# Kernel optimization log

Hardware: AMD Instinct MI355X
Metric: run time of the kernel (lower is better)

Reference implementation:

```python
import jax, jax.numpy as jnp
import numpy as np

B, Q, K, D = 16, 2048, 2048, 128
NEG = -1000000.0  # matches torch module's mask fill value (not -inf)


def setup_inputs() -> dict:
    key = jax.random.key(0)
    kq, kk, kv, kl = jax.random.split(key, 4)
    q = jax.random.normal(kq, (B, Q, D), dtype=jnp.float32)
    k = jax.random.normal(kk, (B, K, D), dtype=jnp.float32)
    v = jax.random.normal(kv, (B, K, D), dtype=jnp.float32)
    valid_lens = jax.random.randint(kl, (B, 1), 0, K, dtype=jnp.int32)
    return {"q": q, "k": k, "v": v, "valid_lens": valid_lens}


def reference(q, k, v, valid_lens):
    d = q.shape[-1]
    # scores: (B, Q, K)
    weight = jnp.einsum('bqd,bkd->bqk', q, k) / jnp.sqrt(jnp.asarray(d, q.dtype))
    # mask: key position j valid iff j < valid_len[b]; broadcast over query dim
    mask = jnp.arange(k.shape[1])[None, None, :] < valid_lens[:, :, None]  # (B,1,K)
    weight = jnp.where(mask, weight, NEG)
    score = jax.nn.softmax(weight, axis=-1)
    return jnp.einsum('bqk,bkv->bqv', score, v)
```

## Files before the change

kernel.cpp:

```cpp
#include <hip/hip_runtime.h>

constexpr int NB = 16;
constexpr int NQ = 2048;
constexpr int NK = 2048;
constexpr int ND = 128;
constexpr int KVBLK = 64;
constexpr int NTILE = NK / KVBLK;
constexpr int TILE_USH = KVBLK * ND;
constexpr float SCALE2 = 0.12751744751442557f;

typedef __attribute__((ext_vector_type(4))) float f4;
typedef __attribute__((ext_vector_type(16))) float f32x16;
typedef __attribute__((ext_vector_type(8))) unsigned short us8;
typedef __attribute__((ext_vector_type(8))) __bf16 bf16x8;
typedef __attribute__((ext_vector_type(4))) unsigned int u32x4;

static __device__ __forceinline__ unsigned short f2bf(float f) {
    unsigned u = __builtin_bit_cast(unsigned, f);
    u += 0x7fffu + ((u >> 16) & 1u);
    return (unsigned short)(u >> 16);
}
static __device__ __forceinline__ f4 splat4(float x) { f4 r = {x,x,x,x}; return r; }

static __device__ __forceinline__ float fexp2(float x) {
    float r;
    asm("v_exp_f32 %0, %1" : "=v"(r) : "v"(x));
    return r;
}

static __device__ __forceinline__ void load_lds16(const unsigned short* g, unsigned short* l) {
    __builtin_amdgcn_global_load_lds(
        (const __attribute__((address_space(1))) void*)g,
        (__attribute__((address_space(3))) void*)l,
        16, 0, 0);
}

static __device__ __forceinline__ unsigned cvt_pk_bf16(float lo, float hi) {
    unsigned r;
    asm("v_cvt_pk_bf16_f32 %0, %1, %2" : "=v"(r) : "v"(lo), "v"(hi));
    return r;
}

__global__ __launch_bounds__(256)
void prep_kv5(const float* __restrict__ kg, const float* __restrict__ vg,
              const int* __restrict__ vlen,
              unsigned short* __restrict__ wk, unsigned short* __restrict__ wvt)
{
    const int b   = blockIdx.y;
    const int t   = blockIdx.x;
    const int kv0 = t * KVBLK;

    {
        const int v = vlen[b];
        const int Leff = (v <= 0) ? NK : v;
        if (kv0 >= Leff) return;
    }

    const int t0  = threadIdx.x;

    __shared__ __align__(16) unsigned short vl[64 * 136];

    {
        const int kv = t0 >> 2;
        const int c  = t0 & 3;
        const float* gp = kg + (size_t)(b * NK + kv0 + kv) * ND + c * 32;
        unsigned short* ob = wk + (size_t)(b * NTILE + t) * TILE_USH;
        #pragma unroll
        for (int g = 0; g < 4; ++g) {
            f4 f0 = *(const f4*)(gp + g * 8);
            f4 f1 = *(const f4*)(gp + g * 8 + 4);
            us8 w;
            #pragma unroll
            for (int i = 0; i < 4; ++i) { w[i] = f2bf(f0[i]); w[i+4] = f2bf(f1[i]); }
            const int d0 = c * 32 + g * 8;
            const int f  = (kv >> 5) * 8 + (d0 >> 4);
            const int off = f * 512 + ((d0 >> 3) & 1) * 256 + (kv & 31) * 8;
            *(us8*)(ob + off) = w;
        }
    }
    {
        const int kv = t0 >> 2;
        const int d0 = (t0 & 3) * 32;
        const float* gp = vg + (size_t)(b * NK + kv0 + kv) * ND + d0;
        unsigned short* lb = &vl[kv * 136 + d0];
        #pragma unroll
        for (int g = 0; g < 4; ++g) {
            f4 f0 = *(const f4*)(gp + g * 8);
            f4 f1 = *(const f4*)(gp + g * 8 + 4);
            us8 w;
            #pragma unroll
            for (int i = 0; i < 4; ++i) { w[i] = f2bf(f0[i]); w[i+4] = f2bf(f1[i]); }
            *(us8*)(lb + g * 8) = w;
        }
    }
    __syncthreads();
    {
        unsigned short* ob = wvt + (size_t)(b * NTILE + t) * TILE_USH;
        #pragma unroll
        for (int iter = 0; iter < 4; ++iter) {
            const int cid = iter * 256 + t0;
            const int f   = cid >> 6;
            const int l   = cid & 63;
            const int kb  = (f >> 2) * 16 + (l >> 5) * 8;
            const int d   = (f & 3) * 32 + (l & 31);
            us8 w;
            #pragma unroll
            for (int j = 0; j < 8; ++j) w[j] = vl[(kb + j) * 136 + d];
            *(us8*)(ob + cid * 8) = w;
        }
    }
}

__global__ __launch_bounds__(256, 2)
void attn_fused14(const float* __restrict__ qg, const int* __restrict__ vlen,
                  const unsigned short* __restrict__ wk,
                  const unsigned short* __restrict__ wvt,
                  float* __restrict__ og)
{
    const int bid  = blockIdx.x;
    const int half = bid >> 8;
    const int j    = bid & 255;
    const int rank = half ? (15 - (j & 7)) : (j & 7);
    const int qc   = j >> 3;
    const int q0   = qc * 64;

    int b = 0;
    {
        int Ls[16];
        #pragma unroll
        for (int i = 0; i < 16; ++i) {
            const int v = vlen[i];
            Ls[i] = (v <= 0) ? NK : v;
        }
        #pragma unroll
        for (int bb = 0; bb < 16; ++bb) {
            int r = 0;
            #pragma unroll
            for (int cc = 0; cc < 16; ++cc)
                r += (Ls[cc] > Ls[bb] || (Ls[cc] == Ls[bb] && cc < bb)) ? 1 : 0;
            if (r == rank) b = bb;
        }
    }

    const int tid  = threadIdx.x;
    const int wid  = tid >> 6;
    const int grp  = wid >> 1;
    const int qw   = wid & 1;
    const int lane = tid & 63;
    const int lq   = lane & 31;
    const int hi   = lane >> 5;

    const int L = vlen[b];
    const bool uniform = (L <= 0);
    const int Leff = uniform ? NK : L;
    const int ntiles = (Leff + KVBLK - 1) / KVBLK;
    const int ng    = (ntiles + 1 - grp) >> 1;
    const int niter = (ntiles + 1) >> 1;

    __shared__ __align__(16) unsigned short smem[2][2 * TILE_USH];

    bf16x8 aq[8];
    {
        const float* qp = qg + (size_t)(b * NQ + q0 + qw * 32 + lq) * ND + hi * 8;
        #pragma unroll
        for (int c = 0; c < 8; ++c) {
            f4 f0 = *(const f4*)(qp + c * 16);
            f4 f1 = *(const f4*)(qp + c * 16 + 4);
            us8 u;
            #pragma unroll
            for (int i = 0; i < 4; ++i) {
                u[i]     = f2bf(f0[i] * SCALE2);
                u[i + 4] = f2bf(f1[i] * SCALE2);
            }
            aq[c] = __builtin_bit_cast(bf16x8, u);
        }
    }

    const unsigned short* kbg = wk  + (size_t)b * NTILE * TILE_USH;
    const unsigned short* vbg = wvt + (size_t)b * NTILE * TILE_USH;

    const unsigned short* sbase = qw ? vbg : kbg;
    unsigned short* sdst = &smem[grp][qw * 8192];
    const int s_off = lane * 8;

    float m_r = -__builtin_inff();
    float l_r = 0.f;
    f32x16 accO[4];
    #pragma unroll
    for (int dc = 0; dc < 4; ++dc)
        #pragma unroll
        for (int r = 0; r < 16; ++r) accO[dc][r] = 0.f;

    if (grp < ntiles) {
        const unsigned short* src = sbase + (size_t)grp * TILE_USH + s_off;
        #pragma unroll
        for (int jj = 0; jj < 16; ++jj) load_lds16(src + jj * 512, sdst + jj * 512);
    }
    __syncthreads();

    for (int i = 0; i < niter; ++i) {
        const int tile = 2 * i + grp;
        const unsigned short* kl  = &smem[grp][0];
        const unsigned short* vl2 = &smem[grp][8192];
        const bool act = (i < ng);

        us8 kf[16], vf[16];
        f32x16 sA, sB;
        if (act) {
            #pragma unroll
            for (int c = 0; c < 16; ++c)
                kf[c] = *(const us8*)&kl[c * 512 + lane * 8];
            #pragma unroll
            for (int r = 0; r < 16; ++r) { sA[r] = 0.f; sB[r] = 0.f; }
            #pragma unroll
            for (int c = 0; c < 8; ++c) {
                sA = __builtin_amdgcn_mfma_f32_32x32x16_bf16(
                    __builtin_bit_cast(bf16x8, kf[c]), aq[c], sA, 0, 0, 0);
                sB = __builtin_amdgcn_mfma_f32_32x32x16_bf16(
                    __builtin_bit_cast(bf16x8, kf[8 + c]), aq[c], sB, 0, 0, 0);
            }
            __builtin_amdgcn_sched_barrier(0);
            #pragma unroll
            for (int f = 0; f < 16; ++f)
                vf[f] = *(const us8*)&vl2[f * 512 + lane * 8];
        }

        __syncthreads();

        {
            const int tn = tile + 2;
            if (tn < ntiles) {
                const unsigned short* src = sbase + (size_t)tn * TILE_USH + s_off;
                #pragma unroll
                for (int jj = 0; jj < 16; ++jj) load_lds16(src + jj * 512, sdst + jj * 512);
            }
        }

        if (act) {
            const int kv0 = tile * KVBLK;

            if (uniform) {
                #pragma unroll
                for (int r = 0; r < 16; ++r) { sA[r] = 0.f; sB[r] = 0.f; }
            } else {
                const int lim0 = L - kv0 - 4 * hi;
                const int lim1 = lim0 - 32;
                #pragma unroll
                for (int r = 0; r < 16; ++r) {
                    const int rc = (r & 3) + 8 * (r >> 2);
                    sA[r] = (rc >= lim0) ? -__builtin_inff() : sA[r];
                    sB[r] = (rc >= lim1) ? -__builtin_inff() : sB[r];
                }
            }

            float mx[8];
            #pragma unroll
            for (int i2 = 0; i2 < 8; ++i2)
                mx[i2] = fmaxf(fmaxf(sA[i2], sA[i2 + 8]), fmaxf(sB[i2], sB[i2 + 8]));
            #pragma unroll
            for (int i2 = 0; i2 < 4; ++i2) mx[i2] = fmaxf(mx[i2], mx[i2 + 4]);
            float pm = fmaxf(fmaxf(mx[0], mx[1]), fmaxf(mx[2], mx[3]));
            float pmax = fmaxf(pm, __shfl_xor(pm, 32));

            if (__any(pmax > m_r)) {
                const float mnew = fmaxf(m_r, pmax);
                const float sc = fexp2(m_r - mnew);
                m_r = mnew;
                l_r *= sc;
                #pragma unroll
                for (int r = 0; r < 16; ++r) {
                    const int src = ((r & 3) + 8 * (r >> 2) + 4 * hi) + (lane & 32);
                    const float scr = __shfl(sc, src);
                    accO[0][r] *= scr; accO[1][r] *= scr;
                    accO[2][r] *= scr; accO[3][r] *= scr;
                }
            }

            float p0[16], p1[16];
            #pragma unroll
            for (int r = 0; r < 16; ++r) {
                p0[r] = fexp2(sA[r] - m_r);
                p1[r] = fexp2(sB[r] - m_r);
            }
            float sm[8];
            #pragma unroll
            for (int i2 = 0; i2 < 8; ++i2)
                sm[i2] = (p0[i2] + p0[i2 + 8]) + (p1[i2] + p1[i2 + 8]);
            #pragma unroll
            for (int i2 = 0; i2 < 4; ++i2) sm[i2] += sm[i2 + 4];
            float rsum = (sm[0] + sm[1]) + (sm[2] + sm[3]);
            rsum += __shfl_xor(rsum, 32);
            l_r += rsum;

            unsigned cw[16];
            #pragma unroll
            for (int i2 = 0; i2 < 8; ++i2) cw[i2] = cvt_pk_bf16(p0[2 * i2], p0[2 * i2 + 1]);
            #pragma unroll
            for (int i2 = 0; i2 < 8; ++i2) cw[8 + i2] = cvt_pk_bf16(p1[2 * i2], p1[2 * i2 + 1]);

            bf16x8 pa[4];
            #pragma unroll
            for (int ks = 0; ks < 4; ++ks) {
                const int a = 4 * ks;
                const unsigned u = hi ? cw[a]     : cw[a + 2];
                const unsigned v = hi ? cw[a + 1] : cw[a + 3];
                const unsigned up = __shfl_xor((int)u, 32);
                const unsigned vp = __shfl_xor((int)v, 32);
                u32x4 w;
                w[0] = hi ? up        : cw[a];
                w[1] = hi ? vp        : cw[a + 1];
                w[2] = hi ? cw[a + 2] : up;
                w[3] = hi ? cw[a + 3] : vp;
                pa[ks] = __builtin_bit_cast(bf16x8, w);
            }

            #pragma unroll
            for (int dc = 0; dc < 4; ++dc) {
                #pragma unroll
                for (int ks = 0; ks < 4; ++ks) {
                    accO[dc] = __builtin_amdgcn_mfma_f32_32x32x16_bf16(
                        pa[ks], __builtin_bit_cast(bf16x8, vf[ks * 4 + dc]), accO[dc], 0, 0, 0);
                }
            }
        }

        __syncthreads();
    }

    float* accb = (float*)&smem[0][0];
    float* mlb  = accb + 8192;
    if (grp == 1) {
        #pragma unroll
        for (int dc = 0; dc < 4; ++dc) {
            #pragma unroll
            for (int q4 = 0; q4 < 4; ++q4) {
                f4 v;
                #pragma unroll
                for (int c = 0; c < 4; ++c) v[c] = accO[dc][q4 * 4 + c];
                *(f4*)&accb[(((qw * 16 + dc * 4 + q4) * 64) + lane) * 4] = v;
            }
        }
        if (hi == 0) {
            mlb[qw * 32 + lq]      = m_r;
            mlb[64 + qw * 32 + lq] = l_r;
        }
    }
    __syncthreads();
    if (grp == 0) {
        const float m1 = mlb[qw * 32 + lq];
        const float l1 = mlb[64 + qw * 32 + lq];
        const float m  = fmaxf(m_r, m1);
        const float a0 = fexp2(m_r - m), a1 = fexp2(m1 - m);
        const float linv = 1.0f / (a0 * l_r + a1 * l1);
        const float s0v = a0 * linv, s1v = a1 * linv;
        float* ob = og + (size_t)(b * NQ + q0 + qw * 32) * ND;
        #pragma unroll
        for (int dc = 0; dc < 4; ++dc) {
            #pragma unroll
            for (int q4 = 0; q4 < 4; ++q4) {
                f4 o1 = *(const f4*)&accb[(((qw * 16 + dc * 4 + q4) * 64) + lane) * 4];
                #pragma unroll
                for (int c = 0; c < 4; ++c) {
                    const int r = q4 * 4 + c;
                    const int row = c + 8 * q4 + 4 * hi;
                    const float s0r = __shfl(s0v, row + (lane & 32));
                    const float s1r = __shfl(s1v, row + (lane & 32));
                    ob[(size_t)row * ND + dc * 32 + lq] = accO[dc][r] * s0r + o1[c] * s1r;
                }
            }
        }
    }
}

__global__ __launch_bounds__(256, 2)
void attn_fused(const float* __restrict__ qg, const float* __restrict__ kg,
                const float* __restrict__ vg, const int* __restrict__ vlen,
                float* __restrict__ og)
{
    const int b    = blockIdx.y;
    const int q0   = blockIdx.x * 64;
    const int tid  = threadIdx.x;
    const int wid  = tid >> 6;
    const int lane = tid & 63;
    const int lrow = lane & 15;
    const int lgrp = lane >> 4;
    constexpr float SCALE = 0.08838834764831844f;

    const int L = vlen[b];
    const bool uniform = (L <= 0);
    const int Leff = uniform ? NK : L;
    const int nt32 = (Leff + 31) / 32;

    __shared__ __align__(16) unsigned short kt[32 * 136];
    __shared__ __align__(16) unsigned short vt[128 * 40];
    __shared__ __align__(16) float pt[4][16 * 36];

    bf16x8 aqf[4];
    {
        const float* qp = qg + (size_t)(b * NQ + q0 + wid * 16 + lrow) * ND + lgrp * 8;
        #pragma unroll
        for (int c = 0; c < 4; ++c) {
            f4 f0 = *(const f4*)(qp + c * 32);
            f4 f1 = *(const f4*)(qp + c * 32 + 4);
            us8 u;
            #pragma unroll
            for (int i = 0; i < 4; ++i) {
                u[i]     = f2bf(f0[i] * SCALE);
                u[i + 4] = f2bf(f1[i] * SCALE);
            }
            aqf[c] = __builtin_bit_cast(bf16x8, u);
        }
    }

    float m_r[4], l_r[4];
    f4 accO[8];
    #pragma unroll
    for (int r = 0; r < 4; ++r) { m_r[r] = -__builtin_inff(); l_r[r] = 0.f; }
    #pragma unroll
    for (int dc = 0; dc < 8; ++dc) accO[dc] = splat4(0.f);

    for (int t = 0; t < nt32; ++t) {
        const int kv0 = t * 32;
        __syncthreads();
        {
            const int r  = tid >> 3;
            const int c0 = (tid & 7) * 16;
            const float* gp = kg + (size_t)(b * NK + kv0 + r) * ND + c0;
            f4 f0 = *(const f4*)(gp);
            f4 f1 = *(const f4*)(gp + 4);
            f4 f2 = *(const f4*)(gp + 8);
            f4 f3 = *(const f4*)(gp + 12);
            us8 w0, w1;
            #pragma unroll
            for (int i = 0; i < 4; ++i) {
                w0[i]     = f2bf(f0[i]);
                w0[i + 4] = f2bf(f1[i]);
                w1[i]     = f2bf(f2[i]);
                w1[i + 4] = f2bf(f3[i]);
            }
            unsigned short* dst = &kt[r * 136 + c0];
            *(us8*)(dst)     = w0;
            *(us8*)(dst + 8) = w1;
        }
        {
            const int d  = tid & 127;
            const int g2 = tid >> 7;
            const float* gp = vg + (size_t)(b * NK + kv0 + g2 * 16) * ND + d;
            us8 w0, w1;
            #pragma unroll
            for (int jj = 0; jj < 8; ++jj) {
                w0[jj] = f2bf(gp[(size_t)jj * ND]);
                w1[jj] = f2bf(gp[(size_t)(jj + 8) * ND]);
            }
            unsigned short* dst = &vt[d * 40 + g2 * 16];
            *(us8*)(dst)     = w0;
            *(us8*)(dst + 8) = w1;
        }
        __syncthreads();

        f4 s0 = splat4(0.f), s1 = splat4(0.f);
        #pragma unroll
        for (int c = 0; c < 4; ++c) {
            bf16x8 bk0 = __builtin_bit_cast(bf16x8,
                *(const us8*)&kt[lrow * 136 + c * 32 + lgrp * 8]);
            s0 = __builtin_amdgcn_mfma_f32_16x16x32_bf16(aqf[c], bk0, s0, 0, 0, 0);
            bf16x8 bk1 = __builtin_bit_cast(bf16x8,
                *(const us8*)&kt[(16 + lrow) * 136 + c * 32 + lgrp * 8]);
            s1 = __builtin_amdgcn_mfma_f32_16x16x32_bf16(aqf[c], bk1, s1, 0, 0, 0);
        }

        const int col0 = kv0 + lrow;
        if (uniform) {
            s0 = splat4(0.f);
            s1 = splat4(0.f);
        } else {
            if (col0 >= L)      s0 = splat4(-__builtin_inff());
            if (col0 + 16 >= L) s1 = splat4(-__builtin_inff());
        }

        float pm[4];
        #pragma unroll
        for (int r = 0; r < 4; ++r) pm[r] = fmaxf(s0[r], s1[r]);
        #pragma unroll
        for (int off = 8; off > 0; off >>= 1) {
            #pragma unroll
            for (int r = 0; r < 4; ++r)
                pm[r] = fmaxf(pm[r], __shfl_xor(pm[r], off));
        }
        float pr0[4], pr1[4], rs[4], sc[4];
        #pragma unroll
        for (int r = 0; r < 4; ++r) {
            float mn = fmaxf(m_r[r], pm[r]);
            sc[r]  = __expf(m_r[r] - mn);
            m_r[r] = mn;
            pr0[r] = __expf(s0[r] - mn);
            pr1[r] = __expf(s1[r] - mn);
            rs[r]  = pr0[r] + pr1[r];
        }
        #pragma unroll
        for (int off = 8; off > 0; off >>= 1) {
            #pragma unroll
            for (int r = 0; r < 4; ++r)
                rs[r] += __shfl_xor(rs[r], off);
        }
        #pragma unroll
        for (int r = 0; r < 4; ++r) l_r[r] = l_r[r] * sc[r] + rs[r];
        #pragma unroll
        for (int dc = 0; dc < 8; ++dc) {
            #pragma unroll
            for (int r = 0; r < 4; ++r) accO[dc][r] *= sc[r];
        }

        float* pw = pt[wid];
        #pragma unroll
        for (int r = 0; r < 4; ++r) {
            pw[(lgrp * 4 + r) * 36 + lrow]      = pr0[r];
            pw[(lgrp * 4 + r) * 36 + 16 + lrow] = pr1[r];
        }
        asm volatile("s_waitcnt lgkmcnt(0)" ::: "memory");
        f4 a0 = *(const f4*)&pw[lrow * 36 + lgrp * 8];
        f4 a1 = *(const f4*)&pw[lrow * 36 + lgrp * 8 + 4];
        us8 au;
        #pragma unroll
        for (int i = 0; i < 4; ++i) { au[i] = f2bf(a0[i]); au[i + 4] = f2bf(a1[i]); }
        bf16x8 ap = __builtin_bit_cast(bf16x8, au);

        #pragma unroll
        for (int dc = 0; dc < 8; ++dc) {
            bf16x8 bv = __builtin_bit_cast(bf16x8,
                *(const us8*)&vt[(dc * 16 + lrow) * 40 + lgrp * 8]);
            accO[dc] = __builtin_amdgcn_mfma_f32_16x16x32_bf16(ap, bv, accO[dc], 0, 0, 0);
        }
    }

    float inv[4];
    #pragma unroll
    for (int r = 0; r < 4; ++r) inv[r] = 1.0f / l_r[r];
    float* op = og + (size_t)(b * NQ + q0 + wid * 16) * ND;
    #pragma unroll
    for (int dc = 0; dc < 8; ++dc) {
        #pragma unroll
        for (int r = 0; r < 4; ++r)
            op[(lgrp * 4 + r) * ND + dc * 16 + lrow] = accO[dc][r] * inv[r];
    }
}

extern "C" void kernel_launch(void* const* d_in, const int* in_sizes, int n_in,
                              void* d_out, int out_size, void* d_ws, size_t ws_size,
                              hipStream_t stream) {
    (void)in_sizes; (void)n_in; (void)out_size;
    const float* q  = (const float*)d_in[0];
    const float* k  = (const float*)d_in[1];
    const float* v  = (const float*)d_in[2];
    const int*   vl = (const int*)d_in[3];
    float* out = (float*)d_out;

    const size_t kvbytes = 2 * (size_t)NB * NK * ND * sizeof(unsigned short);
    if (ws_size >= kvbytes) {
        unsigned short* wk  = (unsigned short*)d_ws;
        unsigned short* wvt = wk + (size_t)NB * NK * ND;
        hipLaunchKernelGGL(prep_kv5, dim3(NTILE, NB), dim3(256), 0, stream, k, v, vl, wk, wvt);
        hipLaunchKernelGGL(attn_fused14, dim3((NQ / 64) * NB), dim3(256), 0, stream,
                           q, vl, wk, wvt, out);
    } else {
        hipLaunchKernelGGL(attn_fused, dim3(NQ / 64, NB), dim3(256), 0, stream,
                           q, k, v, vl, out);
    }
}
```

Before: 57.16 us.

## Split KV tiles into 32-key subtiles with double-buffered LDS and one barrier

Each wave group now processes 32-key subtiles instead of 64-key tiles, and each group gets two LDS buffers so the next subtile's load is issued before computing the current one. The mid-iteration __syncthreads is removed, leaving one barrier per iteration. This aims to overlap global-to-LDS transfers with MFMA work and to shorten the masked tail by trimming work to 32-key granularity. The cost is twice as many iterations, each with a smaller MFMA batch and its own online-softmax rescaling and reductions. The subtile addressing assumes the pre-swizzled K/V tile layout splits cleanly into two halves of 4096 elements.

```diff
diff --git a/kernel.cpp b/kernel.cpp
--- a/kernel.cpp
+++ b/kernel.cpp
@@ -112,7 +112,7 @@
 }
 
 __global__ __launch_bounds__(256, 2)
-void attn_fused14(const float* __restrict__ qg, const int* __restrict__ vlen,
+void attn_fused16(const float* __restrict__ qg, const int* __restrict__ vlen,
                   const unsigned short* __restrict__ wk,
                   const unsigned short* __restrict__ wvt,
                   float* __restrict__ og)
@@ -153,11 +153,11 @@
     const int L = vlen[b];
     const bool uniform = (L <= 0);
     const int Leff = uniform ? NK : L;
-    const int ntiles = (Leff + KVBLK - 1) / KVBLK;
-    const int ng    = (ntiles + 1 - grp) >> 1;
-    const int niter = (ntiles + 1) >> 1;
-
-    __shared__ __align__(16) unsigned short smem[2][2 * TILE_USH];
+    const int nsub = (Leff + 31) >> 5;
+    const int ng    = (nsub > grp) ? ((nsub - grp + 1) >> 1) : 0;
+    const int niter = (nsub + 1) >> 1;
+
+    __shared__ __align__(16) unsigned short smem[2][2][8192];
 
     bf16x8 aq[8];
     {
@@ -180,7 +180,6 @@
     const unsigned short* vbg = wvt + (size_t)b * NTILE * TILE_USH;
 
     const unsigned short* sbase = qw ? vbg : kbg;
-    unsigned short* sdst = &smem[grp][qw * 8192];
     const int s_off = lane * 8;
 
     float m_r = -__builtin_inff();
@@ -191,72 +190,69 @@
         #pragma unroll
         for (int r = 0; r < 16; ++r) accO[dc][r] = 0.f;
 
-    if (grp < ntiles) {
-        const unsigned short* src = sbase + (size_t)grp * TILE_USH + s_off;
-        #pragma unroll
-        for (int jj = 0; jj < 16; ++jj) load_lds16(src + jj * 512, sdst + jj * 512);
+    if (grp < nsub) {
+        const int s = grp;
+        const unsigned short* src =
+            sbase + (size_t)(s >> 1) * TILE_USH + (s & 1) * 4096 + s_off;
+        unsigned short* dst = &smem[grp][0][qw * 4096];
+        #pragma unroll
+        for (int jj = 0; jj < 8; ++jj) load_lds16(src + jj * 512, dst + jj * 512);
     }
     __syncthreads();
 
     for (int i = 0; i < niter; ++i) {
-        const int tile = 2 * i + grp;
-        const unsigned short* kl  = &smem[grp][0];
-        const unsigned short* vl2 = &smem[grp][8192];
-        const bool act = (i < ng);
-
-        us8 kf[16], vf[16];
-        f32x16 sA, sB;
-        if (act) {
-            #pragma unroll
-            for (int c = 0; c < 16; ++c)
+        const int buf = i & 1;
+
+        {
+            const int sn = 2 * (i + 1) + grp;
+            if (sn < nsub) {
+                const unsigned short* src =
+                    sbase + (size_t)(sn >> 1) * TILE_USH + (sn & 1) * 4096 + s_off;
+                unsigned short* dst = &smem[grp][buf ^ 1][qw * 4096];
+                #pragma unroll
+                for (int jj = 0; jj < 8; ++jj) load_lds16(src + jj * 512, dst + jj * 512);
+            }
+        }
+
+        if (i < ng) {
+            const int s   = 2 * i + grp;
+            const int kv0 = s * 32;
+            const unsigned short* kl  = &smem[grp][buf][0];
+            const unsigned short* vl2 = &smem[grp][buf][4096];
+
+            us8 kf[8];
+            #pragma unroll
+            for (int c = 0; c < 8; ++c)
                 kf[c] = *(const us8*)&kl[c * 512 + lane * 8];
-            #pragma unroll
-            for (int r = 0; r < 16; ++r) { sA[r] = 0.f; sB[r] = 0.f; }
-            #pragma unroll
-            for (int c = 0; c < 8; ++c) {
+            f32x16 sA;
+            #pragma unroll
+            for (int r = 0; r < 16; ++r) sA[r] = 0.f;
+            #pragma unroll
+            for (int c = 0; c < 8; ++c)
                 sA = __builtin_amdgcn_mfma_f32_32x32x16_bf16(
                     __builtin_bit_cast(bf16x8, kf[c]), aq[c], sA, 0, 0, 0);
-                sB = __builtin_amdgcn_mfma_f32_32x32x16_bf16(
-                    __builtin_bit_cast(bf16x8, kf[8 + c]), aq[c], sB, 0, 0, 0);
-            }
             __builtin_amdgcn_sched_barrier(0);
-            #pragma unroll
-            for (int f = 0; f < 16; ++f)
+            us8 vf[8];
+            #pragma unroll
+            for (int f = 0; f < 8; ++f)
                 vf[f] = *(const us8*)&vl2[f * 512 + lane * 8];
-        }
-
-        __syncthreads();
-
-        {
-            const int tn = tile + 2;
-            if (tn < ntiles) {
-                const unsigned short* src = sbase + (size_t)tn * TILE_USH + s_off;
-                #pragma unroll
-                for (int jj = 0; jj < 16; ++jj) load_lds16(src + jj * 512, sdst + jj * 512);
-            }
-        }
-
-        if (act) {
-            const int kv0 = tile * KVBLK;
 
             if (uniform) {
                 #pragma unroll
-                for (int r = 0; r < 16; ++r) { sA[r] = 0.f; sB[r] = 0.f; }
+                for (int r = 0; r < 16; ++r) sA[r] = 0.f;
             } else {
                 const int lim0 = L - kv0 - 4 * hi;
-                const int lim1 = lim0 - 32;
                 #pragma unroll
                 for (int r = 0; r < 16; ++r) {
                     const int rc = (r & 3) + 8 * (r >> 2);
                     sA[r] = (rc >= lim0) ? -__builtin_inff() : sA[r];
-                    sB[r] = (rc >= lim1) ? -__builtin_inff() : sB[r];
                 }
             }
 
             float mx[8];
             #pragma unroll
             for (int i2 = 0; i2 < 8; ++i2)
-                mx[i2] = fmaxf(fmaxf(sA[i2], sA[i2 + 8]), fmaxf(sB[i2], sB[i2 + 8]));
+                mx[i2] = fmaxf(sA[i2], sA[i2 + 8]);
             #pragma unroll
             for (int i2 = 0; i2 < 4; ++i2) mx[i2] = fmaxf(mx[i2], mx[i2 + 4]);
             float pm = fmaxf(fmaxf(mx[0], mx[1]), fmaxf(mx[2], mx[3]));
@@ -276,31 +272,25 @@
                 }
             }
 
-            float p0[16], p1[16];
-            #pragma unroll
-            for (int r = 0; r < 16; ++r) {
-                p0[r] = fexp2(sA[r] - m_r);
-                p1[r] = fexp2(sB[r] - m_r);
-            }
+            float p0[16];
+            #pragma unroll
+            for (int r = 0; r < 16; ++r) p0[r] = fexp2(sA[r] - m_r);
             float sm[8];
             #pragma unroll
-            for (int i2 = 0; i2 < 8; ++i2)
-                sm[i2] = (p0[i2] + p0[i2 + 8]) + (p1[i2] + p1[i2 + 8]);
+            for (int i2 = 0; i2 < 8; ++i2) sm[i2] = p0[i2] + p0[i2 + 8];
             #pragma unroll
             for (int i2 = 0; i2 < 4; ++i2) sm[i2] += sm[i2 + 4];
             float rsum = (sm[0] + sm[1]) + (sm[2] + sm[3]);
             rsum += __shfl_xor(rsum, 32);
             l_r += rsum;
 
-            unsigned cw[16];
+            unsigned cw[8];
             #pragma unroll
             for (int i2 = 0; i2 < 8; ++i2) cw[i2] = cvt_pk_bf16(p0[2 * i2], p0[2 * i2 + 1]);
-            #pragma unroll
-            for (int i2 = 0; i2 < 8; ++i2) cw[8 + i2] = cvt_pk_bf16(p1[2 * i2], p1[2 * i2 + 1]);
-
-            bf16x8 pa[4];
-            #pragma unroll
-            for (int ks = 0; ks < 4; ++ks) {
+
+            bf16x8 pa[2];
+            #pragma unroll
+            for (int ks = 0; ks < 2; ++ks) {
                 const int a = 4 * ks;
                 const unsigned u = hi ? cw[a]     : cw[a + 2];
                 const unsigned v = hi ? cw[a + 1] : cw[a + 3];
@@ -317,7 +307,7 @@
             #pragma unroll
             for (int dc = 0; dc < 4; ++dc) {
                 #pragma unroll
-                for (int ks = 0; ks < 4; ++ks) {
+                for (int ks = 0; ks < 2; ++ks) {
                     accO[dc] = __builtin_amdgcn_mfma_f32_32x32x16_bf16(
                         pa[ks], __builtin_bit_cast(bf16x8, vf[ks * 4 + dc]), accO[dc], 0, 0, 0);
                 }
@@ -327,7 +317,7 @@
         __syncthreads();
     }
 
-    float* accb = (float*)&smem[0][0];
+    float* accb = (float*)&smem[0][0][0];
     float* mlb  = accb + 8192;
     if (grp == 1) {
         #pragma unroll
@@ -560,7 +550,7 @@
         unsigned short* wk  = (unsigned short*)d_ws;
         unsigned short* wvt = wk + (size_t)NB * NK * ND;
         hipLaunchKernelGGL(prep_kv5, dim3(NTILE, NB), dim3(256), 0, stream, k, v, vl, wk, wvt);
-        hipLaunchKernelGGL(attn_fused14, dim3((NQ / 64) * NB), dim3(256), 0, stream,
+        hipLaunchKernelGGL(attn_fused16, dim3((NQ / 64) * NB), dim3(256), 0, stream,
                            q, vl, wk, wvt, out);
     } else {
         hipLaunchKernelGGL(attn_fused, dim3(NQ / 64, NB), dim3(256), 0, stream,
```

After: 59.83 us. 4.7% more time.
